# Kernel tuning notes

Measured on AMD Instinct MI355X. Metric: run time of the kernel, lower is better.

The kernel has to match this reference:

```python
import jax, jax.numpy as jnp
import numpy as np

EPS = 1e-6


def _rmsnorm(x, w):
    var = jnp.mean(x * x, axis=-1, keepdims=True)
    return x * jax.lax.rsqrt(var + EPS) * w


def _rotate_half(x):
    h = x.shape[-1] // 2
    return jnp.concatenate([-x[..., h:], x[..., :h]], axis=-1)


def setup_inputs() -> dict:
    key = jax.random.key(0)
    B, T, H = 2, 2048, 2048
    nh, nkv, d = 16, 8, 128
    max_pos = 4096
    ks = jax.random.split(key, 6)
    s = 0.02
    x = jax.random.normal(ks[0], (B, T, H), jnp.float32)
    # real RoPE tables (Qwen3 uses rope_theta=1e6)
    inv_freq = 1.0 / (1e6 ** (np.arange(0, d, 2, dtype=np.float64) / d))
    freqs = np.outer(np.arange(max_pos), inv_freq)
    emb = np.concatenate([freqs, freqs], axis=-1)
    cos = jnp.asarray(np.cos(emb), jnp.float32)
    sin = jnp.asarray(np.sin(emb), jnp.float32)
    position_ids = jnp.broadcast_to(jnp.arange(T, dtype=jnp.int32)[None, :], (B, T))
    Wq = jax.random.normal(ks[1], (nh * d, H), jnp.float32) * s
    Wk = jax.random.normal(ks[2], (nkv * d, H), jnp.float32) * s
    Wv = jax.random.normal(ks[3], (nkv * d, H), jnp.float32) * s
    Wo = jax.random.normal(ks[4], (H, nh * d), jnp.float32) * s
    q_norm_w = jnp.ones((d,), jnp.float32)
    k_norm_w = jnp.ones((d,), jnp.float32)
    return {"x": x, "cos": cos, "sin": sin, "position_ids": position_ids,
            "Wq": Wq, "Wk": Wk, "Wv": Wv, "Wo": Wo,
            "q_norm_w": q_norm_w, "k_norm_w": k_norm_w}


def reference(x, cos, sin, position_ids, Wq, Wk, Wv, Wo, q_norm_w, k_norm_w):
    B, T, H = x.shape
    d = q_norm_w.shape[0]
    nh = Wq.shape[0] // d
    nkv = Wk.shape[0] // d
    groups = nh // nkv

    # QKV projections (F.linear: x @ W.T)
    q = jnp.einsum('bth,oh->bto', x, Wq).reshape(B, T, nh, d).transpose(0, 2, 1, 3)   # [B,nh,T,d]
    k = jnp.einsum('bth,oh->bto', x, Wk).reshape(B, T, nkv, d).transpose(0, 2, 1, 3)  # [B,nkv,T,d]
    v = jnp.einsum('bth,oh->bto', x, Wv).reshape(B, T, nkv, d).transpose(0, 2, 1, 3)

    # per-head RMSNorm on q and k
    q = _rmsnorm(q, q_norm_w)
    k = _rmsnorm(k, k_norm_w)

    # RoPE
    cos_b = cos[position_ids][:, None, :, :]  # [B,1,T,d]
    sin_b = sin[position_ids][:, None, :, :]
    q = q * cos_b + _rotate_half(q) * sin_b
    k = k * cos_b + _rotate_half(k) * sin_b

    # GQA expand (repeat_interleave along head dim)
    if groups > 1:
        k = jnp.repeat(k, groups, axis=1)
        v = jnp.repeat(v, groups, axis=1)

    # causal SDPA
    scale = 1.0 / jnp.sqrt(jnp.asarray(d, x.dtype))
    scores = jnp.einsum('bhqd,bhkd->bhqk', q, k) * scale  # [B,nh,T,T]
    causal = jnp.tril(jnp.ones((T, T), bool))
    scores = jnp.where(causal[None, None], scores, jnp.asarray(-jnp.inf, scores.dtype))
    probs = jax.nn.softmax(scores, axis=-1)
    attn = jnp.einsum('bhqk,bhkd->bhqd', probs, v)  # [B,nh,T,d]

    attn = attn.transpose(0, 2, 1, 3).reshape(B, T, nh * d)
    return jnp.einsum('bto,ho->bth', attn, Wo)
```

## Files before the change

kernel.cpp:

```cpp
#include <hip/hip_runtime.h>
#include <stdint.h>
#include <stddef.h>

typedef unsigned short u16;
typedef __attribute__((ext_vector_type(4))) unsigned short u16x4;
typedef __attribute__((ext_vector_type(8))) short bf16x8;
typedef __attribute__((ext_vector_type(4))) float f32x4;
typedef __attribute__((ext_vector_type(16))) float f32x16;

#define B_   2
#define T_   2048
#define NH   16
#define NKV  8
#define HD   128

__device__ __forceinline__ u16 f2bf(float f) {
  union { float f; uint32_t u; } v; v.f = f;
  uint32_t u = v.u;
  u += 0x7FFFu + ((u >> 16) & 1u);
  return (u16)(u >> 16);
}
__device__ __forceinline__ float bf2f(u16 h) {
  union { uint32_t u; float f; } v; v.u = ((uint32_t)h) << 16;
  return v.f;
}
__device__ __forceinline__ uint32_t cvt_pk_bf16(float lo, float hi) {
  uint32_t r;
  asm("v_cvt_pk_bf16_f32 %0, %1, %2" : "=v"(r) : "v"(lo), "v"(hi));
  return r;
}

__device__ __forceinline__ void gload_lds16(const void* g, void* l) {
  __builtin_amdgcn_global_load_lds(
      (__attribute__((address_space(1))) void*)g,
      (__attribute__((address_space(3))) void*)l, 16, 0, 0);
}

__global__ __launch_bounds__(256) void cvt_f32_bf16(const float* __restrict__ in,
                                                    u16* __restrict__ out, int n4) {
  int i = blockIdx.x * 256 + threadIdx.x;
  if (i >= n4) return;
  float4 v = reinterpret_cast<const float4*>(in)[i];
  u16x4 o;
  o.x = f2bf(v.x); o.y = f2bf(v.y); o.z = f2bf(v.z); o.w = f2bf(v.w);
  reinterpret_cast<u16x4*>(out)[i] = o;
}

template<int BM, int BN, int STORE>
__global__ __launch_bounds__(512, 2) void gemm2(const u16* __restrict__ A,
                                                const u16* __restrict__ Bm,
                                                void* __restrict__ C0,
                                                void* __restrict__ C1,
                                                void* __restrict__ C2,
                                                int M, int N, int K) {
  constexpr int FM  = BM / 32;
  constexpr int FN  = BN / 64;
  constexpr int ASZ = BM * 64;
  constexpr int BSZ = BN * 64;
  __shared__ u16 lds[2 * (ASZ + BSZ)];

  const int tid  = threadIdx.x;
  const int lane = tid & 63;
  const int wid  = tid >> 6;
  const int lr   = lane & 15;
  const int lg   = lane >> 4;
  const int wm0 = (wid >> 2) * (BM / 2);
  const int wn0 = (wid & 3) * (BN / 4);

  const int s  = ((blockIdx.x & 7) << 5) | (blockIdx.x >> 3);
  const int nx = N / BN;
  const int m0 = (s / nx) * BM;
  const int n0 = (s % nx) * BN;

  f32x4 acc[FM][FN];
#pragma unroll
  for (int i = 0; i < FM; ++i)
#pragma unroll
    for (int j = 0; j < FN; ++j) acc[i][j] = (f32x4){0.f, 0.f, 0.f, 0.f};

  auto stage = [&](int kt, int p) {
    const int k0 = kt << 6;
    u16* Ab = lds + p * (ASZ + BSZ);
    u16* Bb = Ab + ASZ;
#pragma unroll
    for (int it = 0; it < BM / 64; ++it) {
      const int CI = it * 512 + tid;
      const int row = CI >> 3, c = CI & 7;
      gload_lds16(A + (size_t)(m0 + row) * K + k0 + ((c ^ (row & 7)) << 3),
                  (char*)Ab + (size_t)CI * 16);
    }
#pragma unroll
    for (int it = 0; it < BN / 64; ++it) {
      const int CI = it * 512 + tid;
      const int row = CI >> 3, c = CI & 7;
      gload_lds16(Bm + (size_t)(n0 + row) * K + k0 + ((c ^ (row & 7)) << 3),
                  (char*)Bb + (size_t)CI * 16);
    }
  };

  const int nk = K >> 6;
  stage(0, 0);
  __syncthreads();
  int cur = 0;
  for (int kt = 0; kt < nk; ++kt) {
    if (kt + 1 < nk) stage(kt + 1, cur ^ 1);
    const u16* Ab = lds + cur * (ASZ + BSZ);
    const u16* Bb = Ab + ASZ;
#pragma unroll
    for (int kk = 0; kk < 2; ++kk) {
      bf16x8 af[FM], bfr[FN];
#pragma unroll
      for (int mt = 0; mt < FM; ++mt) {
        const int ar = wm0 + mt * 16 + lr;
        af[mt] = *reinterpret_cast<const bf16x8*>(
            (const char*)Ab + ar * 128 + ((kk * 64 + lg * 16) ^ ((ar & 7) << 4)));
      }
#pragma unroll
      for (int nt = 0; nt < FN; ++nt) {
        const int br = wn0 + nt * 16 + lr;
        bfr[nt] = *reinterpret_cast<const bf16x8*>(
            (const char*)Bb + br * 128 + ((kk * 64 + lg * 16) ^ ((br & 7) << 4)));
      }
      __builtin_amdgcn_s_setprio(1);
#pragma unroll
      for (int mt = 0; mt < FM; ++mt)
#pragma unroll
        for (int nt = 0; nt < FN; ++nt)
          acc[mt][nt] = __builtin_amdgcn_mfma_f32_16x16x32_bf16(
              af[mt], bfr[nt], acc[mt][nt], 0, 0, 0);
      __builtin_amdgcn_s_setprio(0);
    }
    __syncthreads();
    cur ^= 1;
  }

  if (STORE == 3) {
    u16* Qd = (u16*)C0; u16* Kd = (u16*)C1; u16* Vd = (u16*)C2;
    if (n0 < 2048) {
#pragma unroll
      for (int mt = 0; mt < FM; ++mt) {
        const int row = m0 + wm0 + mt * 16 + lg * 4;
#pragma unroll
        for (int nt = 0; nt < FN; ++nt) {
          const int col = n0 + wn0 + nt * 16 + lr;
#pragma unroll
          for (int r = 0; r < 4; ++r)
            Qd[(size_t)(row + r) * 2048 + col] = f2bf(acc[mt][nt][r]);
        }
      }
    } else if (n0 < 3072) {
#pragma unroll
      for (int mt = 0; mt < FM; ++mt) {
        const int row = m0 + wm0 + mt * 16 + lg * 4;
#pragma unroll
        for (int nt = 0; nt < FN; ++nt) {
          const int col = n0 + wn0 + nt * 16 + lr - 2048;
#pragma unroll
          for (int r = 0; r < 4; ++r)
            Kd[(size_t)(row + r) * 1024 + col] = f2bf(acc[mt][nt][r]);
        }
      }
    } else {
#pragma unroll
      for (int mt = 0; mt < FM; ++mt) {
        const int row = m0 + wm0 + mt * 16 + lg * 4;
        const int b = row >> 11;
        const int t = row & (T_ - 1);
#pragma unroll
        for (int nt = 0; nt < FN; ++nt) {
          const int vc = n0 + wn0 + nt * 16 + lr - 3072;
          u16x4 v;
          v.x = f2bf(acc[mt][nt][0]); v.y = f2bf(acc[mt][nt][1]);
          v.z = f2bf(acc[mt][nt][2]); v.w = f2bf(acc[mt][nt][3]);
          *reinterpret_cast<u16x4*>(Vd + ((size_t)(b * 1024 + vc)) * T_ + t) = v;
        }
      }
    }
  } else {
    float* C = (float*)C0;
#pragma unroll
    for (int mt = 0; mt < FM; ++mt) {
      const int row = m0 + wm0 + mt * 16 + lg * 4;
#pragma unroll
      for (int nt = 0; nt < FN; ++nt) {
        const int col = n0 + wn0 + nt * 16 + lr;
#pragma unroll
        for (int r = 0; r < 4; ++r)
          C[(size_t)(row + r) * N + col] = acc[mt][nt][r];
      }
    }
  }
}

__global__ __launch_bounds__(256) void rms_rope(u16* __restrict__ Q, u16* __restrict__ Kb,
                                                const float* __restrict__ cosT,
                                                const float* __restrict__ sinT,
                                                const int* __restrict__ pos,
                                                const float* __restrict__ qw,
                                                const float* __restrict__ kw) {
  const int wave = blockIdx.x * 4 + (threadIdx.x >> 6);
  const int lane = threadIdx.x & 63;
  const int bt = wave & (B_ * T_ - 1);
  const int hh = wave >> 12;
  u16* ptr;
  const float* w;
  if (hh < NH) { ptr = Q + (size_t)bt * (NH * HD) + hh * HD; w = qw; }
  else         { ptr = Kb + (size_t)bt * (NKV * HD) + (hh - NH) * HD; w = kw; }
  const int p = pos[bt];

  float e0 = bf2f(ptr[lane]);
  float e1 = bf2f(ptr[lane + 64]);
  float ss = e0 * e0 + e1 * e1;
#pragma unroll
  for (int off = 1; off < 64; off <<= 1) ss += __shfl_xor(ss, off, 64);
  const float r = rsqrtf(ss * (1.0f / 128.0f) + 1e-6f);
  const float n0 = e0 * r * w[lane];
  const float n1 = e1 * r * w[lane + 64];
  const float c0 = cosT[(size_t)p * HD + lane], c1 = cosT[(size_t)p * HD + lane + 64];
  const float s0 = sinT[(size_t)p * HD + lane], s1 = sinT[(size_t)p * HD + lane + 64];
  ptr[lane]      = f2bf(n0 * c0 - n1 * s0);
  ptr[lane + 64] = f2bf(n1 * c1 + n0 * s1);
}

__global__ __launch_bounds__(256, 2) void flash_attn3(const u16* __restrict__ Qw,
                                                      const u16* __restrict__ Kw,
                                                      const u16* __restrict__ VTw,
                                                      u16* __restrict__ Ow) {
  __shared__ __align__(16) char smem[65536];

  const int tid  = threadIdx.x;
  const int lane = tid & 63;
  const int wid  = tid >> 6;
  const int rl   = lane & 31;
  const int hi   = lane >> 5;
  const int blk  = blockIdx.x;
  const int qtr = blk >> 5;
  const int qt  = (blk < 256) ? (15 - qtr) : (qtr - 8);
  const int bh  = blk & 31;
  const int b   = bh >> 4, h = bh & 15, kvh = h >> 1;
  const int q0w = qt * 128 + wid * 32;
  const int qg  = q0w + rl;
  const int swz = (rl & 7) << 4;

  bf16x8 qf[8];
  {
    const u16* qp = Qw + ((size_t)(b * T_) + qg) * (NH * HD) + h * HD + hi * 8;
#pragma unroll
    for (int kd = 0; kd < 8; ++kd) qf[kd] = *reinterpret_cast<const bf16x8*>(qp + kd * 16);
  }

  f32x16 ot[4];
#pragma unroll
  for (int dt = 0; dt < 4; ++dt)
#pragma unroll
    for (int r = 0; r < 16; ++r) ot[dt][r] = 0.f;
  float m = -1e30f, lsum = 0.f;
  const float scale = 0.08838834764831845f;

  auto stageKV = [&](int kt, int p) {
    char* Kb = smem + p * 32768;
    char* Vb = Kb + 16384;
    {
      const int row = tid >> 4, ch = tid & 15;
#pragma unroll
      for (int it = 0; it < 4; ++it) {
        const int rr = it * 16 + row;
        const int scol = ((ch * 16) ^ ((rr & 7) << 4)) >> 1;
        gload_lds16(Kw + ((size_t)(b * T_) + kt * 64 + rr) * (NKV * HD) + kvh * HD + scol,
                    Kb + (it * 256 + tid) * 16);
      }
    }
    {
      const int row = tid >> 3, ch = tid & 7;
#pragma unroll
      for (int it = 0; it < 4; ++it) {
        const int rr = it * 32 + row;
        const int scol = ((ch * 16) ^ ((rr & 7) << 4)) >> 1;
        gload_lds16(VTw + ((size_t)((b * NKV + kvh) * HD) + rr) * T_ + kt * 64 + scol,
                    Vb + (it * 256 + tid) * 16);
      }
    }
  };

  const int nkt = 2 * qt + 2;
  stageKV(0, 0);
  __syncthreads();
  for (int kt = 0; kt < nkt; ++kt) {
    const int cur = kt & 1;
    if (kt + 1 < nkt) stageKV(kt + 1, cur ^ 1);

    if (64 * kt <= q0w + 31) {
      const u16* Kb = (const u16*)(smem + cur * 32768);
      const u16* Vb = (const u16*)(smem + cur * 32768 + 16384);

      f32x16 s0, s1;
#pragma unroll
      for (int r = 0; r < 16; ++r) { s0[r] = 0.f; s1[r] = 0.f; }
      __builtin_amdgcn_s_setprio(1);
#pragma unroll
      for (int kd = 0; kd < 8; ++kd) {
        const int cb = (kd * 32 + hi * 16) ^ swz;
        const bf16x8 k0 = *reinterpret_cast<const bf16x8*>((const char*)Kb + rl * 256 + cb);
        const bf16x8 k1 = *reinterpret_cast<const bf16x8*>((const char*)Kb + (32 + rl) * 256 + cb);
        s0 = __builtin_amdgcn_mfma_f32_32x32x16_bf16(k0, qf[kd], s0, 0, 0, 0);
        s1 = __builtin_amdgcn_mfma_f32_32x32x16_bf16(k1, qf[kd], s1, 0, 0, 0);
      }
      __builtin_amdgcn_s_setprio(0);

      const int kv0 = kt * 64;
      const bool maskT = (kv0 + 63 > q0w);
      float rm = -1e30f;
#pragma unroll
      for (int r = 0; r < 16; ++r) {
        const int cr = (r & 3) + 8 * (r >> 2) + 4 * hi;
        float a = s0[r] * scale, c = s1[r] * scale;
        if (maskT) {
          if (kv0 + cr > qg)      a = -1e30f;
          if (kv0 + 32 + cr > qg) c = -1e30f;
        }
        s0[r] = a; s1[r] = c;
        rm = fmaxf(rm, fmaxf(a, c));
      }
      rm = fmaxf(rm, __shfl_xor(rm, 32));
      const float mn = fmaxf(m, rm);
      const float al = __expf(m - mn);
      m = mn;
      float rs = 0.f;
#pragma unroll
      for (int r = 0; r < 16; ++r) {
        const float p0 = __expf(s0[r] - mn);
        const float p1 = __expf(s1[r] - mn);
        s0[r] = p0; s1[r] = p1;
        rs += p0 + p1;
      }
      rs += __shfl_xor(rs, 32);
      lsum = lsum * al + rs;
#pragma unroll
      for (int dt = 0; dt < 4; ++dt)
#pragma unroll
        for (int r = 0; r < 16; ++r) ot[dt][r] *= al;

      bf16x8 pf[2][2];
#pragma unroll
      for (int ks = 0; ks < 2; ++ks) {
        {
          uint32_t X0 = cvt_pk_bf16(s0[8 * ks + 0], s0[8 * ks + 1]);
          uint32_t X1 = cvt_pk_bf16(s0[8 * ks + 2], s0[8 * ks + 3]);
          uint32_t Y0 = cvt_pk_bf16(s0[8 * ks + 4], s0[8 * ks + 5]);
          uint32_t Y1 = cvt_pk_bf16(s0[8 * ks + 6], s0[8 * ks + 7]);
          asm volatile("v_permlane32_swap_b32 %0, %1" : "+v"(X0), "+v"(Y0));
          asm volatile("v_permlane32_swap_b32 %0, %1" : "+v"(X1), "+v"(Y1));
          union { uint32_t w[4]; bf16x8 v; } u;
          u.w[0] = X0; u.w[1] = X1; u.w[2] = Y0; u.w[3] = Y1;
          pf[0][ks] = u.v;
        }
        {
          uint32_t X0 = cvt_pk_bf16(s1[8 * ks + 0], s1[8 * ks + 1]);
          uint32_t X1 = cvt_pk_bf16(s1[8 * ks + 2], s1[8 * ks + 3]);
          uint32_t Y0 = cvt_pk_bf16(s1[8 * ks + 4], s1[8 * ks + 5]);
          uint32_t Y1 = cvt_pk_bf16(s1[8 * ks + 6], s1[8 * ks + 7]);
          asm volatile("v_permlane32_swap_b32 %0, %1" : "+v"(X0), "+v"(Y0));
          asm volatile("v_permlane32_swap_b32 %0, %1" : "+v"(X1), "+v"(Y1));
          union { uint32_t w[4]; bf16x8 v; } u;
          u.w[0] = X0; u.w[1] = X1; u.w[2] = Y0; u.w[3] = Y1;
          pf[1][ks] = u.v;
        }
      }

      __builtin_amdgcn_s_setprio(1);
#pragma unroll
      for (int dt = 0; dt < 4; ++dt) {
        const int rv = dt * 32 + rl;
#pragma unroll
        for (int kvc = 0; kvc < 2; ++kvc)
#pragma unroll
          for (int ks = 0; ks < 2; ++ks) {
            const int cb = (kvc * 64 + ks * 32 + hi * 16) ^ swz;
            const bf16x8 vf = *reinterpret_cast<const bf16x8*>((const char*)Vb + rv * 128 + cb);
            ot[dt] = __builtin_amdgcn_mfma_f32_32x32x16_bf16(vf, pf[kvc][ks], ot[dt], 0, 0, 0);
          }
      }
      __builtin_amdgcn_s_setprio(0);
    }
    __syncthreads();
  }

  const float inv = 1.0f / lsum;
  u16* ep = (u16*)smem + wid * (32 * 136);
#pragma unroll
  for (int dt = 0; dt < 4; ++dt)
#pragma unroll
    for (int r = 0; r < 16; ++r) {
      const int d = dt * 32 + (r & 3) + 8 * (r >> 2) + 4 * hi;
      ep[rl * 136 + d] = f2bf(ot[dt][r] * inv);
    }
  const int dh = hi * 64;
  const u16* srcp = (u16*)smem + wid * (32 * 136) + rl * 136 + dh;
  u16* gdst = Ow + ((size_t)(b * T_) + q0w + rl) * (NH * HD) + h * HD + dh;
#pragma unroll
  for (int c2 = 0; c2 < 8; ++c2)
    *reinterpret_cast<bf16x8*>(gdst + c2 * 8) =
        *reinterpret_cast<const bf16x8*>(srcp + c2 * 8);
}

extern "C" void kernel_launch(void* const* d_in, const int* in_sizes, int n_in,
                              void* d_out, int out_size, void* d_ws, size_t ws_size,
                              hipStream_t stream) {
  (void)in_sizes; (void)n_in; (void)out_size; (void)ws_size;
  const float* x    = (const float*)d_in[0];
  const float* cosT = (const float*)d_in[1];
  const float* sinT = (const float*)d_in[2];
  const int*   pos  = (const int*)d_in[3];
  const float* Wq   = (const float*)d_in[4];
  const float* Wk   = (const float*)d_in[5];
  const float* Wv   = (const float*)d_in[6];
  const float* Wo   = (const float*)d_in[7];
  const float* qw   = (const float*)d_in[8];
  const float* kw   = (const float*)d_in[9];
  float* out = (float*)d_out;

  char* ws = (char*)d_ws;
  u16* xb   = (u16*)(ws + 0);
  u16* Wqb  = (u16*)(ws + 16777216);
  u16* Wkb  = (u16*)(ws + 25165824);
  u16* Wvb  = (u16*)(ws + 29360128);
  u16* Wob  = (u16*)(ws + 33554432);
  u16* Qws  = (u16*)(ws + 41943040);
  u16* Kws  = (u16*)(ws + 58720256);
  u16* VTws = (u16*)(ws + 67108864);
  u16* Aws  = (u16*)(ws + 75497472);

  cvt_f32_bf16<<<8192, 256, 0, stream>>>(x,  xb,  2097152);
  cvt_f32_bf16<<<4096, 256, 0, stream>>>(Wq, Wqb, 1048576);
  cvt_f32_bf16<<<2048, 256, 0, stream>>>(Wk, Wkb, 524288);
  cvt_f32_bf16<<<2048, 256, 0, stream>>>(Wv, Wvb, 524288);
  cvt_f32_bf16<<<4096, 256, 0, stream>>>(Wo, Wob, 1048576);

  gemm2<256, 256, 3><<<256, 512, 0, stream>>>(xb, Wqb, Qws, Kws, VTws,
                                              4096, 4096, 2048);

  rms_rope<<<24576, 256, 0, stream>>>(Qws, Kws, cosT, sinT, pos, qw, kw);

  flash_attn3<<<512, 256, 0, stream>>>(Qws, Kws, VTws, Aws);

  gemm2<128, 256, 2><<<256, 512, 0, stream>>>(Aws, Wob, out, nullptr, nullptr,
                                              4096, 2048, 2048);
}
```

Baseline: 206.9 us.

## Fold softmax scale into Q, use exp2, lazy rescale, wider LDS swizzle

Pre-multiplies Q by scale*log2(e) in the rms_rope kernel, so attention can use the raw v_exp_f32 (exp2) and skip the per-element scale multiply. The running max is now updated only when the new block max exceeds the old one by more than a threshold, which avoids rescaling the output accumulator on most iterations. The mask loop is split into masked and unmasked paths, and the K/V LDS layout uses a 16-way XOR swizzle with paired V rows to cut bank conflicts. Folding the scale into Q, which is stored as bf16, changes rounding slightly. The lazy rescale lets exp2 arguments reach about 2^11.5, so fp32 sums grow larger before normalisation.

```diff
diff --git a/kernel.cpp b/kernel.cpp
--- a/kernel.cpp
+++ b/kernel.cpp
@@ -14,6 +14,8 @@
 #define NKV  8
 #define HD   128
 
+#define QSCALE 0.1275174457f
+
 __device__ __forceinline__ u16 f2bf(float f) {
   union { float f; uint32_t u; } v; v.f = f;
   uint32_t u = v.u;
@@ -27,6 +29,11 @@
 __device__ __forceinline__ uint32_t cvt_pk_bf16(float lo, float hi) {
   uint32_t r;
   asm("v_cvt_pk_bf16_f32 %0, %1, %2" : "=v"(r) : "v"(lo), "v"(hi));
+  return r;
+}
+__device__ __forceinline__ float fexp2(float x) {
+  float r;
+  asm("v_exp_f32 %0, %1" : "=v"(r) : "v"(x));
   return r;
 }
 
@@ -204,8 +211,9 @@
   const int hh = wave >> 12;
   u16* ptr;
   const float* w;
-  if (hh < NH) { ptr = Q + (size_t)bt * (NH * HD) + hh * HD; w = qw; }
-  else         { ptr = Kb + (size_t)bt * (NKV * HD) + (hh - NH) * HD; w = kw; }
+  float post;
+  if (hh < NH) { ptr = Q + (size_t)bt * (NH * HD) + hh * HD; w = qw; post = QSCALE; }
+  else         { ptr = Kb + (size_t)bt * (NKV * HD) + (hh - NH) * HD; w = kw; post = 1.0f; }
   const int p = pos[bt];
 
   float e0 = bf2f(ptr[lane]);
@@ -213,7 +221,7 @@
   float ss = e0 * e0 + e1 * e1;
 #pragma unroll
   for (int off = 1; off < 64; off <<= 1) ss += __shfl_xor(ss, off, 64);
-  const float r = rsqrtf(ss * (1.0f / 128.0f) + 1e-6f);
+  const float r = rsqrtf(ss * (1.0f / 128.0f) + 1e-6f) * post;
   const float n0 = e0 * r * w[lane];
   const float n1 = e1 * r * w[lane + 64];
   const float c0 = cosT[(size_t)p * HD + lane], c1 = cosT[(size_t)p * HD + lane + 64];
@@ -222,7 +230,7 @@
   ptr[lane + 64] = f2bf(n1 * c1 + n0 * s1);
 }
 
-__global__ __launch_bounds__(256, 2) void flash_attn3(const u16* __restrict__ Qw,
+__global__ __launch_bounds__(256, 2) void flash_attn4(const u16* __restrict__ Qw,
                                                       const u16* __restrict__ Kw,
                                                       const u16* __restrict__ VTw,
                                                       u16* __restrict__ Ow) {
@@ -240,7 +248,7 @@
   const int b   = bh >> 4, h = bh & 15, kvh = h >> 1;
   const int q0w = qt * 128 + wid * 32;
   const int qg  = q0w + rl;
-  const int swz = (rl & 7) << 4;
+  const int kswz = (rl & 15) << 4;
 
   bf16x8 qf[8];
   {
@@ -255,30 +263,27 @@
 #pragma unroll
     for (int r = 0; r < 16; ++r) ot[dt][r] = 0.f;
   float m = -1e30f, lsum = 0.f;
-  const float scale = 0.08838834764831845f;
 
   auto stageKV = [&](int kt, int p) {
     char* Kb = smem + p * 32768;
     char* Vb = Kb + 16384;
-    {
-      const int row = tid >> 4, ch = tid & 15;
-#pragma unroll
-      for (int it = 0; it < 4; ++it) {
-        const int rr = it * 16 + row;
-        const int scol = ((ch * 16) ^ ((rr & 7) << 4)) >> 1;
-        gload_lds16(Kw + ((size_t)(b * T_) + kt * 64 + rr) * (NKV * HD) + kvh * HD + scol,
-                    Kb + (it * 256 + tid) * 16);
-      }
-    }
-    {
-      const int row = tid >> 3, ch = tid & 7;
-#pragma unroll
-      for (int it = 0; it < 4; ++it) {
-        const int rr = it * 32 + row;
-        const int scol = ((ch * 16) ^ ((rr & 7) << 4)) >> 1;
-        gload_lds16(VTw + ((size_t)((b * NKV + kvh) * HD) + rr) * T_ + kt * 64 + scol,
-                    Vb + (it * 256 + tid) * 16);
-      }
+#pragma unroll
+    for (int it = 0; it < 4; ++it) {
+      const int CI = it * 256 + tid;
+      const int row = CI >> 4;
+      const int Wp = ((CI & 15) << 4) ^ ((row & 15) << 4);
+      gload_lds16(Kw + ((size_t)(b * T_) + kt * 64 + row) * (NKV * HD) + kvh * HD + (Wp >> 1),
+                  Kb + (size_t)CI * 16);
+    }
+#pragma unroll
+    for (int it = 0; it < 4; ++it) {
+      const int CI = it * 256 + tid;
+      const int sup = CI >> 4;
+      const int Wp = ((CI & 15) << 4) ^ ((sup & 15) << 4);
+      const int d   = sup * 2 + (Wp >> 7);
+      const int kvb = Wp & 127;
+      gload_lds16(VTw + ((size_t)((b * NKV + kvh) * HD) + d) * T_ + kt * 64 + (kvb >> 1),
+                  Vb + (size_t)CI * 16);
     }
   };
 
@@ -299,7 +304,7 @@
       __builtin_amdgcn_s_setprio(1);
 #pragma unroll
       for (int kd = 0; kd < 8; ++kd) {
-        const int cb = (kd * 32 + hi * 16) ^ swz;
+        const int cb = (kd * 32 + hi * 16) ^ kswz;
         const bf16x8 k0 = *reinterpret_cast<const bf16x8*>((const char*)Kb + rl * 256 + cb);
         const bf16x8 k1 = *reinterpret_cast<const bf16x8*>((const char*)Kb + (32 + rl) * 256 + cb);
         s0 = __builtin_amdgcn_mfma_f32_32x32x16_bf16(k0, qf[kd], s0, 0, 0, 0);
@@ -310,35 +315,52 @@
       const int kv0 = kt * 64;
       const bool maskT = (kv0 + 63 > q0w);
       float rm = -1e30f;
-#pragma unroll
-      for (int r = 0; r < 16; ++r) {
-        const int cr = (r & 3) + 8 * (r >> 2) + 4 * hi;
-        float a = s0[r] * scale, c = s1[r] * scale;
-        if (maskT) {
+      if (maskT) {
+#pragma unroll
+        for (int r = 0; r < 16; ++r) {
+          const int cr = (r & 3) + 8 * (r >> 2) + 4 * hi;
+          float a = s0[r], c = s1[r];
           if (kv0 + cr > qg)      a = -1e30f;
           if (kv0 + 32 + cr > qg) c = -1e30f;
-        }
-        s0[r] = a; s1[r] = c;
-        rm = fmaxf(rm, fmaxf(a, c));
+          s0[r] = a; s1[r] = c;
+          rm = fmaxf(rm, fmaxf(a, c));
+        }
+      } else {
+#pragma unroll
+        for (int r = 0; r < 16; ++r) rm = fmaxf(rm, fmaxf(s0[r], s1[r]));
       }
       rm = fmaxf(rm, __shfl_xor(rm, 32));
-      const float mn = fmaxf(m, rm);
-      const float al = __expf(m - mn);
-      m = mn;
-      float rs = 0.f;
-#pragma unroll
-      for (int r = 0; r < 16; ++r) {
-        const float p0 = __expf(s0[r] - mn);
-        const float p1 = __expf(s1[r] - mn);
-        s0[r] = p0; s1[r] = p1;
-        rs += p0 + p1;
-      }
-      rs += __shfl_xor(rs, 32);
-      lsum = lsum * al + rs;
-#pragma unroll
-      for (int dt = 0; dt < 4; ++dt)
-#pragma unroll
-        for (int r = 0; r < 16; ++r) ot[dt][r] *= al;
+
+      if (__all(rm <= m + 11.5f)) {
+        float rs = 0.f;
+#pragma unroll
+        for (int r = 0; r < 16; ++r) {
+          const float p0 = fexp2(s0[r] - m);
+          const float p1 = fexp2(s1[r] - m);
+          s0[r] = p0; s1[r] = p1;
+          rs += p0 + p1;
+        }
+        rs += __shfl_xor(rs, 32);
+        lsum += rs;
+      } else {
+        const float mn = fmaxf(m, rm);
+        const float al = fexp2(m - mn);
+        m = mn;
+        float rs = 0.f;
+#pragma unroll
+        for (int r = 0; r < 16; ++r) {
+          const float p0 = fexp2(s0[r] - mn);
+          const float p1 = fexp2(s1[r] - mn);
+          s0[r] = p0; s1[r] = p1;
+          rs += p0 + p1;
+        }
+        rs += __shfl_xor(rs, 32);
+        lsum = lsum * al + rs;
+#pragma unroll
+        for (int dt = 0; dt < 4; ++dt)
+#pragma unroll
+          for (int r = 0; r < 16; ++r) ot[dt][r] *= al;
+      }
 
       bf16x8 pf[2][2];
 #pragma unroll
@@ -370,13 +392,18 @@
       __builtin_amdgcn_s_setprio(1);
 #pragma unroll
       for (int dt = 0; dt < 4; ++dt) {
-        const int rv = dt * 32 + rl;
+        const int rv  = dt * 32 + rl;
+        const int sup = rv >> 1;
+        const int vbase = sup * 256;
+        const int vsz   = (sup & 15) << 4;
+        const int in7   = (rv & 1) << 7;
 #pragma unroll
         for (int kvc = 0; kvc < 2; ++kvc)
 #pragma unroll
           for (int ks = 0; ks < 2; ++ks) {
-            const int cb = (kvc * 64 + ks * 32 + hi * 16) ^ swz;
-            const bf16x8 vf = *reinterpret_cast<const bf16x8*>((const char*)Vb + rv * 128 + cb);
+            const int inner = in7 | (kvc * 64 + ks * 32 + hi * 16);
+            const bf16x8 vf = *reinterpret_cast<const bf16x8*>(
+                (const char*)Vb + vbase + (inner ^ vsz));
             ot[dt] = __builtin_amdgcn_mfma_f32_32x32x16_bf16(vf, pf[kvc][ks], ot[dt], 0, 0, 0);
           }
       }
@@ -441,7 +468,7 @@
 
   rms_rope<<<24576, 256, 0, stream>>>(Qws, Kws, cosT, sinT, pos, qw, kw);
 
-  flash_attn3<<<512, 256, 0, stream>>>(Qws, Kws, VTws, Aws);
+  flash_attn4<<<512, 256, 0, stream>>>(Qws, Kws, VTws, Aws);
 
   gemm2<128, 256, 2><<<256, 512, 0, stream>>>(Aws, Wob, out, nullptr, nullptr,
                                               4096, 2048, 2048);
```

New measurement: 280.1 us. 1.35x slower.
